# Performance work log

Hardware: AMD Instinct MI355X
Metric: run time of the kernel (lower is better)

The kernel has to match this reference:

```python
import jax, jax.numpy as jnp
import numpy as np

DIM = 512
N_LABELS = 64


def setup_inputs() -> dict:
    key = jax.random.key(0)
    k1, k2, k3, k4 = jax.random.split(key, 4)
    head = jax.random.normal(k1, (8, 512, DIM), dtype=jnp.float32)
    dep = jax.random.normal(k2, (8, 512, DIM), dtype=jnp.float32)
    label_W = jax.random.normal(k3, (N_LABELS, 2 * DIM), dtype=jnp.float32) * 0.02
    label_b = jax.random.normal(k4, (N_LABELS,), dtype=jnp.float32) * 0.02
    return {"head": head, "dep": dep, "label_W": label_W, "label_b": label_b}


def reference(head, dep, label_W, label_b):
    # Original: concated[b, i*S+j] = concat(head[b,i], dep[b,j]) -> [B, S*S, 2D]
    #           out = (label_W @ concated^T).view(B, L, S, S) + b
    # Fused biaffine decomposition: out[b,l,i,j] = Wh[l].head[b,i] + Wd[l].dep[b,j] + b[l]
    D = head.shape[-1]
    W_head = label_W[:, :D]   # [L, D]
    W_dep = label_W[:, D:]    # [L, D]
    h = jnp.einsum('bid,ld->bli', head, W_head)  # [B, L, S]
    d = jnp.einsum('bjd,ld->blj', dep, W_dep)    # [B, L, S]
    out = h[:, :, :, None] + d[:, :, None, :] + label_b[None, :, None, None]
    return out  # [B, L, S, S]
```

## Files before the change

kernel.cpp:

```cpp
#include <hip/hip_runtime.h>
#include <hip/hip_bf16.h>

#define BATCH 8
#define SEQ   512
#define DIM   512
#define NL    64

typedef float f32x4 __attribute__((ext_vector_type(4)));

__global__ __launch_bounds__(256) void alab_proj2(
    const float* __restrict__ head, const float* __restrict__ dep,
    const float* __restrict__ W, const float* __restrict__ bias,
    float* __restrict__ hbuf, float* __restrict__ dbuf)
{
    __shared__ float4 srow[16][129];
    const int bid   = blockIdx.x;
    const int hd    = bid & 1;
    const int itile = (bid >> 1) & 31;
    const int b     = bid >> 6;
    const int i0    = itile * 16;

    const float* src  = hd ? dep  : head;
    float*       dst  = hd ? dbuf : hbuf;
    const int    wofs = hd ? 128  : 0;

    const float4* s4 = (const float4*)(src + ((size_t)b * SEQ + i0) * DIM);
    #pragma unroll
    for (int u = threadIdx.x; u < 16 * 128; u += 256)
        srow[u >> 7][u & 127] = s4[u];
    __syncthreads();

    const int lane = threadIdx.x & 63;
    const int w    = threadIdx.x >> 6;
    const int i    = lane & 15;
    const int li   = lane >> 4;
    const int lb   = w * 16 + li * 4;

    const f32x4* W4 = (const f32x4*)W;
    f32x4 a0 = {0.f,0.f,0.f,0.f}, a1 = {0.f,0.f,0.f,0.f};
    f32x4 a2 = {0.f,0.f,0.f,0.f}, a3 = {0.f,0.f,0.f,0.f};

    #pragma unroll 4
    for (int k4 = 0; k4 < 128; ++k4) {
        const f32x4 hv = *(const f32x4*)&srow[i][k4];
        const size_t wb = (size_t)lb * 256 + wofs + k4;
        a0 += hv * W4[wb];
        a1 += hv * W4[wb + 256];
        a2 += hv * W4[wb + 512];
        a3 += hv * W4[wb + 768];
    }

    float r[4] = { a0.x + a0.y + a0.z + a0.w,
                   a1.x + a1.y + a1.z + a1.w,
                   a2.x + a2.y + a2.z + a2.w,
                   a3.x + a3.y + a3.z + a3.w };
    #pragma unroll
    for (int s = 0; s < 4; ++s) {
        const int l = lb + s;
        const float v = r[s] + (hd ? 0.f : bias[l]);
        dst[((size_t)b * NL + l) * SEQ + i0 + i] = v;
    }
}

__global__ __launch_bounds__(256) void alab_bcast4(
    const float* __restrict__ hbuf, const float* __restrict__ dbuf,
    float* __restrict__ out)
{
    __shared__ float sh[SEQ];
    __shared__ f32x4 sd4[SEQ / 4];
    const int t  = threadIdx.x;
    const int bl = blockIdx.x;

    sh[t]                  = hbuf[(size_t)bl * SEQ + t];
    sh[t + 256]            = hbuf[(size_t)bl * SEQ + t + 256];
    ((float*)sd4)[t]       = dbuf[(size_t)bl * SEQ + t];
    ((float*)sd4)[t + 256] = dbuf[(size_t)bl * SEQ + t + 256];
    __syncthreads();

    const int j4 = t & 127;
    const int rh = t >> 7;
    const f32x4 dreg = sd4[j4];
    f32x4* ob = (f32x4*)out + (size_t)bl * SEQ * (SEQ / 4);

    #pragma unroll 8
    for (int ii = 0; ii < SEQ; ii += 2) {
        const int i = ii + rh;
        ob[(size_t)i * (SEQ / 4) + j4] = dreg + sh[i];
    }
}

extern "C" void kernel_launch(void* const* d_in, const int* in_sizes, int n_in,
                              void* d_out, int out_size, void* d_ws, size_t ws_size,
                              hipStream_t stream) {
    const float* head = (const float*)d_in[0];
    const float* dep  = (const float*)d_in[1];
    const float* W    = (const float*)d_in[2];
    const float* bias = (const float*)d_in[3];
    float* out  = (float*)d_out;
    float* hbuf = (float*)d_ws;
    float* dbuf = hbuf + (size_t)BATCH * NL * SEQ;

    alab_proj2<<<BATCH * 32 * 2, 256, 0, stream>>>(head, dep, W, bias, hbuf, dbuf);
    alab_bcast4<<<BATCH * NL, 256, 0, stream>>>(hbuf, dbuf, out);
}
```

Baseline: 132.8 us.

## Pre-transpose label weights and remap projection threads to labels for coalesced loads

Adds a small kernel that rewrites the label weights into a k-major [hd][k4][label] float4 layout in workspace. The projection kernel now maps each lane to one label and each wave to four sequence rows, so weight loads across a wave become contiguous and the shared-memory reads of the row tile become wave-uniform broadcasts. Outputs are written as one float4 per lane. This costs an extra kernel launch and a weight round trip through workspace, and it assumes the workspace is large enough for the transposed copy.

```diff
diff --git a/kernel.cpp b/kernel.cpp
--- a/kernel.cpp
+++ b/kernel.cpp
@@ -8,23 +8,32 @@
 
 typedef float f32x4 __attribute__((ext_vector_type(4)));
 
-__global__ __launch_bounds__(256) void alab_proj2(
+__global__ __launch_bounds__(256) void alab_wt(
+    const float* __restrict__ W, f32x4* __restrict__ wt4)
+{
+    const int tid = blockIdx.x * 256 + threadIdx.x;
+    const int l   = tid & 63;
+    const int k4  = (tid >> 6) & 127;
+    const int hd  = tid >> 13;
+    wt4[tid] = *(const f32x4*)(W + (size_t)l * (2 * DIM) + hd * DIM + k4 * 4);
+}
+
+__global__ __launch_bounds__(256) void alab_proj4(
     const float* __restrict__ head, const float* __restrict__ dep,
-    const float* __restrict__ W, const float* __restrict__ bias,
+    const f32x4* __restrict__ wt4, const float* __restrict__ bias,
     float* __restrict__ hbuf, float* __restrict__ dbuf)
 {
-    __shared__ float4 srow[16][129];
+    __shared__ f32x4 srow[16][128];
     const int bid   = blockIdx.x;
     const int hd    = bid & 1;
     const int itile = (bid >> 1) & 31;
     const int b     = bid >> 6;
     const int i0    = itile * 16;
 
-    const float* src  = hd ? dep  : head;
-    float*       dst  = hd ? dbuf : hbuf;
-    const int    wofs = hd ? 128  : 0;
+    const float* src = hd ? dep  : head;
+    float*       dst = hd ? dbuf : hbuf;
 
-    const float4* s4 = (const float4*)(src + ((size_t)b * SEQ + i0) * DIM);
+    const f32x4* s4 = (const f32x4*)(src + ((size_t)b * SEQ + i0) * DIM);
     #pragma unroll
     for (int u = threadIdx.x; u < 16 * 128; u += 256)
         srow[u >> 7][u & 127] = s4[u];
@@ -32,34 +41,23 @@
 
     const int lane = threadIdx.x & 63;
     const int w    = threadIdx.x >> 6;
-    const int i    = lane & 15;
-    const int li   = lane >> 4;
-    const int lb   = w * 16 + li * 4;
 
-    const f32x4* W4 = (const f32x4*)W;
-    f32x4 a0 = {0.f,0.f,0.f,0.f}, a1 = {0.f,0.f,0.f,0.f};
-    f32x4 a2 = {0.f,0.f,0.f,0.f}, a3 = {0.f,0.f,0.f,0.f};
-
+    const f32x4* wbase = wt4 + (size_t)hd * 128 * 64 + lane;
+    f32x4 a0 = {0,0,0,0}, a1 = {0,0,0,0}, a2 = {0,0,0,0}, a3 = {0,0,0,0};
     #pragma unroll 4
     for (int k4 = 0; k4 < 128; ++k4) {
-        const f32x4 hv = *(const f32x4*)&srow[i][k4];
-        const size_t wb = (size_t)lb * 256 + wofs + k4;
-        a0 += hv * W4[wb];
-        a1 += hv * W4[wb + 256];
-        a2 += hv * W4[wb + 512];
-        a3 += hv * W4[wb + 768];
+        const f32x4 wt = wbase[(size_t)k4 * 64];
+        a0 += srow[w * 4 + 0][k4] * wt;
+        a1 += srow[w * 4 + 1][k4] * wt;
+        a2 += srow[w * 4 + 2][k4] * wt;
+        a3 += srow[w * 4 + 3][k4] * wt;
     }
-
-    float r[4] = { a0.x + a0.y + a0.z + a0.w,
-                   a1.x + a1.y + a1.z + a1.w,
-                   a2.x + a2.y + a2.z + a2.w,
-                   a3.x + a3.y + a3.z + a3.w };
-    #pragma unroll
-    for (int s = 0; s < 4; ++s) {
-        const int l = lb + s;
-        const float v = r[s] + (hd ? 0.f : bias[l]);
-        dst[((size_t)b * NL + l) * SEQ + i0 + i] = v;
-    }
+    const float bb = hd ? 0.f : bias[lane];
+    f32x4 r = { a0.x + a0.y + a0.z + a0.w + bb,
+                a1.x + a1.y + a1.z + a1.w + bb,
+                a2.x + a2.y + a2.z + a2.w + bb,
+                a3.x + a3.y + a3.z + a3.w + bb };
+    *(f32x4*)(dst + ((size_t)b * NL + lane) * SEQ + i0 + w * 4) = r;
 }
 
 __global__ __launch_bounds__(256) void alab_bcast4(
@@ -96,10 +94,14 @@
     const float* dep  = (const float*)d_in[1];
     const float* W    = (const float*)d_in[2];
     const float* bias = (const float*)d_in[3];
-    float* out  = (float*)d_out;
+    float* out = (float*)d_out;
+
+    const size_t P = (size_t)BATCH * NL * SEQ;
     float* hbuf = (float*)d_ws;
-    float* dbuf = hbuf + (size_t)BATCH * NL * SEQ;
+    float* dbuf = hbuf + P;
+    f32x4* wt4  = (f32x4*)(dbuf + P);
 
-    alab_proj2<<<BATCH * 32 * 2, 256, 0, stream>>>(head, dep, W, bias, hbuf, dbuf);
+    alab_wt   <<<64,         256, 0, stream>>>(W, wt4);
+    alab_proj4<<<BATCH * 64, 256, 0, stream>>>(head, dep, wt4, bias, hbuf, dbuf);
     alab_bcast4<<<BATCH * NL, 256, 0, stream>>>(hbuf, dbuf, out);
 }
```

Result: faster. 119.6 us (-9.9%).
